# Optimization experiments

Measured on AMD Instinct MI355X. Metric: run time of the kernel, lower is better.

## Reference

```python
import jax, jax.numpy as jnp
import numpy as np

D_MODEL = 768
NUM_HEADS = 12
HEAD_DIM = D_MODEL // NUM_HEADS


def setup_inputs() -> dict:
    key = jax.random.key(0)
    ks = jax.random.split(key, 5)
    B, T = 2, 4096
    x = jax.random.normal(ks[0], (B, T, D_MODEL), dtype=jnp.float32)
    s_in = 1.0 / np.sqrt(D_MODEL)
    W_attn = jax.random.normal(ks[1], (D_MODEL, 3 * D_MODEL), dtype=jnp.float32) * s_in
    b_attn = jnp.zeros((3 * D_MODEL,), dtype=jnp.float32)
    W_proj = jax.random.normal(ks[2], (D_MODEL, D_MODEL), dtype=jnp.float32) * s_in
    b_proj = jnp.zeros((D_MODEL,), dtype=jnp.float32)
    return {"x": x, "W_attn": W_attn, "b_attn": b_attn, "W_proj": W_proj, "b_proj": b_proj}


def reference(x, W_attn, b_attn, W_proj, b_proj):
    B, T, C = x.shape
    H, D = NUM_HEADS, HEAD_DIM
    qkv = x @ W_attn + b_attn                      # [B,T,3C]
    q, k, v = jnp.split(qkv, 3, axis=-1)
    q = q.reshape(B, T, H, D).transpose(0, 2, 1, 3)  # [B,H,T,D]
    k = k.reshape(B, T, H, D).transpose(0, 2, 1, 3)
    v = v.reshape(B, T, H, D).transpose(0, 2, 1, 3)
    scores = jnp.einsum('bhqd,bhkd->bhqk', q, k) / jnp.sqrt(jnp.float32(D))
    attn = jax.nn.softmax(scores, axis=-1)          # [B,H,T,T]
    out = jnp.einsum('bhqk,bhkd->bhqd', attn, v)    # [B,H,T,D]
    out = out.transpose(0, 2, 1, 3).reshape(B, T, C)
    return out @ W_proj + b_proj
```

## Files before the change

### kernel.cpp

```cpp
#include <hip/hip_runtime.h>
#include <cstdint>
#include <cstddef>

#define DEV static __device__ __forceinline__

typedef __attribute__((ext_vector_type(8))) short bf16x8;
typedef __attribute__((ext_vector_type(4))) float f32x4;
typedef __attribute__((ext_vector_type(16))) float f32x16;

#define T_SEQ 4096
#define CDIM  768
#define NH    12
#define HD    64
#define NBH   24
#define M_ROWS 8192

#define OFF_XB   0ull
#define OFF_WAT  (OFF_XB  + (size_t)M_ROWS * CDIM * 2)
#define OFF_WPT  (OFF_WAT + (size_t)(3*CDIM) * CDIM * 2)
#define OFF_Q    (OFF_WPT + (size_t)CDIM * CDIM * 2)
#define OFF_K    (OFF_Q   + (size_t)NBH * T_SEQ * HD * 2)
#define OFF_VT   (OFF_K   + (size_t)NBH * T_SEQ * HD * 2)
#define OFF_O    (OFF_VT  + (size_t)NBH * HD * T_SEQ * 2)

DEV unsigned short f2bf(float f) {
  unsigned u = __builtin_bit_cast(unsigned, f);
  u += 0x7FFFu + ((u >> 16) & 1u);
  return (unsigned short)(u >> 16);
}

DEV void gld_lds16(const void* g, void* l) {
  __builtin_amdgcn_global_load_lds(
      (const __attribute__((address_space(1))) void*)g,
      (__attribute__((address_space(3))) void*)l, 16, 0, 0);
}

DEV void cvt8(const f32x16& s, unsigned* w) {
  asm("v_cvt_pk_bf16_f32 %0, %8, %9\n\t"
      "v_cvt_pk_bf16_f32 %1, %10, %11\n\t"
      "v_cvt_pk_bf16_f32 %2, %12, %13\n\t"
      "v_cvt_pk_bf16_f32 %3, %14, %15\n\t"
      "v_cvt_pk_bf16_f32 %4, %16, %17\n\t"
      "v_cvt_pk_bf16_f32 %5, %18, %19\n\t"
      "v_cvt_pk_bf16_f32 %6, %20, %21\n\t"
      "v_cvt_pk_bf16_f32 %7, %22, %23\n\t"
      "s_nop 3"
      : "=&v"(w[0]), "=&v"(w[1]), "=&v"(w[2]), "=&v"(w[3]),
        "=&v"(w[4]), "=&v"(w[5]), "=&v"(w[6]), "=&v"(w[7])
      : "v"(s[0]), "v"(s[1]), "v"(s[2]), "v"(s[3]),
        "v"(s[4]), "v"(s[5]), "v"(s[6]), "v"(s[7]),
        "v"(s[8]), "v"(s[9]), "v"(s[10]), "v"(s[11]),
        "v"(s[12]), "v"(s[13]), "v"(s[14]), "v"(s[15]));
}

__global__ __launch_bounds__(256) void k_conv(const float* __restrict__ in,
                                              unsigned short* __restrict__ out) {
  int i = blockIdx.x * 256 + threadIdx.x;
  const float4* p = (const float4*)in;
  float4 a = p[i * 2], b = p[i * 2 + 1];
  uint4 o;
  o.x = (unsigned)f2bf(a.x) | ((unsigned)f2bf(a.y) << 16);
  o.y = (unsigned)f2bf(a.z) | ((unsigned)f2bf(a.w) << 16);
  o.z = (unsigned)f2bf(b.x) | ((unsigned)f2bf(b.y) << 16);
  o.w = (unsigned)f2bf(b.z) | ((unsigned)f2bf(b.w) << 16);
  ((uint4*)out)[i] = o;
}

__global__ __launch_bounds__(256) void k_transpose(const float* __restrict__ in,
                                                   unsigned short* __restrict__ out,
                                                   int R, int C) {
  __shared__ float tile[64][65];
  int c0 = blockIdx.x * 64, r0 = blockIdx.y * 64;
  int tid = threadIdx.x;
  for (int i = tid; i < 4096; i += 256) {
    int r = i >> 6, c = i & 63;
    tile[r][c] = in[(size_t)(r0 + r) * C + c0 + c];
  }
  __syncthreads();
  for (int i = tid; i < 4096; i += 256) {
    int c = i >> 6, r = i & 63;
    out[(size_t)(c0 + c) * R + r0 + r] = f2bf(tile[r][c]);
  }
}

__global__ __launch_bounds__(256) void k_qkv(const unsigned short* __restrict__ A,
                                             const unsigned short* __restrict__ Bt,
                                             const float* __restrict__ bias,
                                             unsigned short* __restrict__ Qo,
                                             unsigned short* __restrict__ Ko,
                                             unsigned short* __restrict__ Vt) {
  __shared__ short As[128 * 64];
  __shared__ short Bs[128 * 64];
  const int tid = threadIdx.x;
  const int wave = tid >> 6, lane = tid & 63;
  const int wr = wave >> 1, wc = wave & 1;
  const int m0 = blockIdx.y * 128, n0 = blockIdx.x * 128;

  f32x4 acc[4][4] = {};

#pragma unroll 1
  for (int k0 = 0; k0 < 768; k0 += 64) {
#pragma unroll
    for (int it = 0; it < 4; ++it) {
      int chunk = wave * 4 + it;
      int slot = chunk * 64 + lane;
      int row = slot >> 3, j = slot & 7;
      int kcol = k0 + ((j ^ (row & 7)) << 3);
      gld_lds16(A  + (size_t)(m0 + row) * 768 + kcol, &As[chunk * 512]);
      gld_lds16(Bt + (size_t)(n0 + row) * 768 + kcol, &Bs[chunk * 512]);
    }
    __syncthreads();
#pragma unroll
    for (int kk = 0; kk < 2; ++kk) {
      bf16x8 af[4], bfr[4];
      int cbl = kk * 4 + (lane >> 4);
#pragma unroll
      for (int mi = 0; mi < 4; ++mi) {
        int row = wr * 64 + mi * 16 + (lane & 15);
        af[mi] = *(const bf16x8*)&As[(row * 8 + (cbl ^ (row & 7))) * 8];
      }
#pragma unroll
      for (int ni = 0; ni < 4; ++ni) {
        int row = wc * 64 + ni * 16 + (lane & 15);
        bfr[ni] = *(const bf16x8*)&Bs[(row * 8 + (cbl ^ (row & 7))) * 8];
      }
#pragma unroll
      for (int mi = 0; mi < 4; ++mi)
#pragma unroll
        for (int ni = 0; ni < 4; ++ni)
          acc[mi][ni] = __builtin_amdgcn_mfma_f32_16x16x32_bf16(af[mi], bfr[ni], acc[mi][ni], 0, 0, 0);
    }
    __syncthreads();
  }

  const int which = n0 / 768;
#pragma unroll
  for (int ni = 0; ni < 4; ++ni) {
    int col = n0 + wc * 64 + ni * 16 + (lane & 15);
    int nr = col - which * 768;
    int h = nr >> 6, d = nr & 63;
    float bi = bias[col];
#pragma unroll
    for (int mi = 0; mi < 4; ++mi) {
      int mt = m0 + wr * 64 + mi * 16 + ((lane >> 4) << 2);
      int b = mt >> 12, t = mt & 4095;
      size_t bh = (size_t)(b * NH + h);
#pragma unroll
      for (int r = 0; r < 4; ++r) {
        float v = acc[mi][ni][r] + bi;
        if (which == 0) {
          Qo[bh * (T_SEQ * HD) + (size_t)(t + r) * HD + d] = f2bf(v * 0.18033688011112042f);
        } else if (which == 1) {
          Ko[bh * (T_SEQ * HD) + (size_t)(t + r) * HD + d] = f2bf(v);
        } else {
          int tc = t + r;
          int pc = (tc & ~12) | ((tc & 4) << 1) | ((tc & 8) >> 1);
          Vt[bh * (T_SEQ * HD) + (size_t)d * T_SEQ + pc] = f2bf(v);
        }
      }
    }
  }
}

__global__ __launch_bounds__(256, 3) void k_attn(const unsigned short* __restrict__ Q,
                                                 const unsigned short* __restrict__ K,
                                                 const unsigned short* __restrict__ Vt,
                                                 unsigned short* __restrict__ O) {
  __shared__ char ldsb[2][16384];
  const int tid = threadIdx.x, wave = tid >> 6, lane = tid & 63;
  const int hi = lane >> 5, l31 = lane & 31;
  const int qt = blockIdx.x, bh = blockIdx.y;
  const int b = bh / NH, h = bh % NH;
  const size_t base = (size_t)bh * T_SEQ * HD;
  const int q0 = qt * 128 + wave * 32;

  bf16x8 aq[4];
#pragma unroll
  for (int t = 0; t < 4; ++t)
    aq[t] = *(const bf16x8*)&Q[base + (size_t)(q0 + l31) * HD + t * 16 + hi * 8];

  int koff[4];
#pragma unroll
  for (int t = 0; t < 4; ++t)
    koff[t] = l31 * 128 + ((((t << 1) | hi) ^ (l31 & 7)) << 4);
  int voff[2][2];
#pragma unroll
  for (int kb = 0; kb < 2; ++kb)
#pragma unroll
    for (int ks = 0; ks < 2; ++ks)
      voff[kb][ks] = ((((kb << 2) | (ks << 1) | hi) ^ (l31 & 7)) << 4) + l31 * 128;

  f32x16 oacc0 = {}, oacc1 = {}, lacc = {};
  union { unsigned u[4]; bf16x8 v; } onesf;
  onesf.u[0] = 0x3F803F80u; onesf.u[1] = 0x3F803F80u;
  onesf.u[2] = 0x3F803F80u; onesf.u[3] = 0x3F803F80u;

  auto STAGE = [&](int bufi, int k0) {
#pragma unroll
    for (int it = 0; it < 2; ++it) {
      int chunk = wave * 2 + it;
      int slot = chunk * 64 + lane;
      int row = slot >> 3, j = slot & 7;
      int ce = ((j ^ (row & 7)) << 3);
      gld_lds16(K  + base + (size_t)(k0 + row) * HD + ce, ldsb[bufi] + chunk * 1024);
      gld_lds16(Vt + base + (size_t)row * T_SEQ + k0 + ce, ldsb[bufi] + 8192 + chunk * 1024);
    }
  };

  STAGE(0, 0);
  __syncthreads();

  int buf = 0;
#pragma unroll 1
  for (int kt = 0; kt < 64; ++kt) {
    if (kt < 63) STAGE(buf ^ 1, (kt + 1) * 64);
    const char* Lp = ldsb[buf];
    const char* Vp = Lp + 8192;

    f32x16 s0 = {};
#pragma unroll
    for (int t = 0; t < 4; ++t) {
      bf16x8 kf = *(const bf16x8*)(Lp + koff[t]);
      s0 = __builtin_amdgcn_mfma_f32_32x32x16_bf16(kf, aq[t], s0, 0, 0, 0);
    }
#pragma unroll
    for (int r = 0; r < 16; ++r) s0[r] = __builtin_amdgcn_exp2f(s0[r]);
    unsigned w0[8];
    cvt8(s0, w0);
    union { unsigned u[4]; bf16x8 v; } pf00, pf01;
    pf00.u[0] = w0[0]; pf00.u[1] = w0[1]; pf00.u[2] = w0[2]; pf00.u[3] = w0[3];
    pf01.u[0] = w0[4]; pf01.u[1] = w0[5]; pf01.u[2] = w0[6]; pf01.u[3] = w0[7];

    f32x16 s1 = {};
#pragma unroll
    for (int t = 0; t < 4; ++t) {
      bf16x8 kf = *(const bf16x8*)(Lp + 4096 + koff[t]);
      s1 = __builtin_amdgcn_mfma_f32_32x32x16_bf16(kf, aq[t], s1, 0, 0, 0);
    }

    lacc = __builtin_amdgcn_mfma_f32_32x32x16_bf16(pf00.v, onesf.v, lacc, 0, 0, 0);
    lacc = __builtin_amdgcn_mfma_f32_32x32x16_bf16(pf01.v, onesf.v, lacc, 0, 0, 0);
    {
      bf16x8 v0 = *(const bf16x8*)(Vp + voff[0][0]);
      bf16x8 v1 = *(const bf16x8*)(Vp + voff[0][1]);
      bf16x8 u0 = *(const bf16x8*)(Vp + 4096 + voff[0][0]);
      bf16x8 u1 = *(const bf16x8*)(Vp + 4096 + voff[0][1]);
      oacc0 = __builtin_amdgcn_mfma_f32_32x32x16_bf16(pf00.v, v0, oacc0, 0, 0, 0);
      oacc0 = __builtin_amdgcn_mfma_f32_32x32x16_bf16(pf01.v, v1, oacc0, 0, 0, 0);
      oacc1 = __builtin_amdgcn_mfma_f32_32x32x16_bf16(pf00.v, u0, oacc1, 0, 0, 0);
      oacc1 = __builtin_amdgcn_mfma_f32_32x32x16_bf16(pf01.v, u1, oacc1, 0, 0, 0);
    }

#pragma unroll
    for (int r = 0; r < 16; ++r) s1[r] = __builtin_amdgcn_exp2f(s1[r]);
    unsigned w1[8];
    cvt8(s1, w1);
    union { unsigned u[4]; bf16x8 v; } pf10, pf11;
    pf10.u[0] = w1[0]; pf10.u[1] = w1[1]; pf10.u[2] = w1[2]; pf10.u[3] = w1[3];
    pf11.u[0] = w1[4]; pf11.u[1] = w1[5]; pf11.u[2] = w1[6]; pf11.u[3] = w1[7];

    lacc = __builtin_amdgcn_mfma_f32_32x32x16_bf16(pf10.v, onesf.v, lacc, 0, 0, 0);
    lacc = __builtin_amdgcn_mfma_f32_32x32x16_bf16(pf11.v, onesf.v, lacc, 0, 0, 0);
    {
      bf16x8 v0 = *(const bf16x8*)(Vp + voff[1][0]);
      bf16x8 v1 = *(const bf16x8*)(Vp + voff[1][1]);
      bf16x8 u0 = *(const bf16x8*)(Vp + 4096 + voff[1][0]);
      bf16x8 u1 = *(const bf16x8*)(Vp + 4096 + voff[1][1]);
      oacc0 = __builtin_amdgcn_mfma_f32_32x32x16_bf16(pf10.v, v0, oacc0, 0, 0, 0);
      oacc0 = __builtin_amdgcn_mfma_f32_32x32x16_bf16(pf11.v, v1, oacc0, 0, 0, 0);
      oacc1 = __builtin_amdgcn_mfma_f32_32x32x16_bf16(pf10.v, u0, oacc1, 0, 0, 0);
      oacc1 = __builtin_amdgcn_mfma_f32_32x32x16_bf16(pf11.v, u1, oacc1, 0, 0, 0);
    }

    __syncthreads();
    buf ^= 1;
  }

#pragma unroll
  for (int r = 0; r < 16; ++r) {
    float inv = 1.0f / lacc[r];
    int t = q0 + ((r & 3) + 8 * (r >> 2)) + 4 * hi;
    size_t rowb = (size_t)(b * T_SEQ + t) * CDIM + h * 64;
    O[rowb + l31]      = f2bf(oacc0[r] * inv);
    O[rowb + 32 + l31] = f2bf(oacc1[r] * inv);
  }
}

__global__ __launch_bounds__(256) void k_proj(const unsigned short* __restrict__ A,
                                              const unsigned short* __restrict__ Bt,
                                              const float* __restrict__ bias,
                                              float* __restrict__ out) {
  __shared__ short As[128 * 64];
  __shared__ short Bs[128 * 64];
  const int tid = threadIdx.x;
  const int wave = tid >> 6, lane = tid & 63;
  const int wr = wave >> 1, wc = wave & 1;
  const int m0 = blockIdx.y * 128, n0 = blockIdx.x * 128;

  f32x4 acc[4][4] = {};

#pragma unroll 1
  for (int k0 = 0; k0 < 768; k0 += 64) {
#pragma unroll
    for (int it = 0; it < 4; ++it) {
      int chunk = wave * 4 + it;
      int slot = chunk * 64 + lane;
      int row = slot >> 3, j = slot & 7;
      int kcol = k0 + ((j ^ (row & 7)) << 3);
      gld_lds16(A  + (size_t)(m0 + row) * 768 + kcol, &As[chunk * 512]);
      gld_lds16(Bt + (size_t)(n0 + row) * 768 + kcol, &Bs[chunk * 512]);
    }
    __syncthreads();
#pragma unroll
    for (int kk = 0; kk < 2; ++kk) {
      bf16x8 af[4], bfr[4];
      int cbl = kk * 4 + (lane >> 4);
#pragma unroll
      for (int mi = 0; mi < 4; ++mi) {
        int row = wr * 64 + mi * 16 + (lane & 15);
        af[mi] = *(const bf16x8*)&As[(row * 8 + (cbl ^ (row & 7))) * 8];
      }
#pragma unroll
      for (int ni = 0; ni < 4; ++ni) {
        int row = wc * 64 + ni * 16 + (lane & 15);
        bfr[ni] = *(const bf16x8*)&Bs[(row * 8 + (cbl ^ (row & 7))) * 8];
      }
#pragma unroll
      for (int mi = 0; mi < 4; ++mi)
#pragma unroll
        for (int ni = 0; ni < 4; ++ni)
          acc[mi][ni] = __builtin_amdgcn_mfma_f32_16x16x32_bf16(af[mi], bfr[ni], acc[mi][ni], 0, 0, 0);
    }
    __syncthreads();
  }

#pragma unroll
  for (int ni = 0; ni < 4; ++ni) {
    int col = n0 + wc * 64 + ni * 16 + (lane & 15);
    float bi = bias[col];
#pragma unroll
    for (int mi = 0; mi < 4; ++mi) {
      int mt = m0 + wr * 64 + mi * 16 + ((lane >> 4) << 2);
#pragma unroll
      for (int r = 0; r < 4; ++r)
        out[(size_t)(mt + r) * CDIM + col] = acc[mi][ni][r] + bi;
    }
  }
}

extern "C" void kernel_launch(void* const* d_in, const int* in_sizes, int n_in,
                              void* d_out, int out_size, void* d_ws, size_t ws_size,
                              hipStream_t stream) {
  const float* x  = (const float*)d_in[0];
  const float* Wa = (const float*)d_in[1];
  const float* ba = (const float*)d_in[2];
  const float* Wp = (const float*)d_in[3];
  const float* bp = (const float*)d_in[4];

  char* ws = (char*)d_ws;
  unsigned short* xb  = (unsigned short*)(ws + OFF_XB);
  unsigned short* WaT = (unsigned short*)(ws + OFF_WAT);
  unsigned short* WpT = (unsigned short*)(ws + OFF_WPT);
  unsigned short* Qb  = (unsigned short*)(ws + OFF_Q);
  unsigned short* Kb  = (unsigned short*)(ws + OFF_K);
  unsigned short* Vtb = (unsigned short*)(ws + OFF_VT);
  unsigned short* Ob  = (unsigned short*)(ws + OFF_O);

  k_conv<<<3072, 256, 0, stream>>>(x, xb);
  k_transpose<<<dim3(36, 12), 256, 0, stream>>>(Wa, WaT, CDIM, 3 * CDIM);
  k_transpose<<<dim3(12, 12), 256, 0, stream>>>(Wp, WpT, CDIM, CDIM);
  k_qkv<<<dim3(18, 64), 256, 0, stream>>>(xb, WaT, ba, Qb, Kb, Vtb);
  k_attn<<<dim3(32, 24), 256, 0, stream>>>(Qb, Kb, Vtb, Ob);
  k_proj<<<dim3(6, 64), 256, 0, stream>>>(Ob, WpT, bp, (float*)d_out);
}
```

Baseline: 229.5 us.

## Replace MFMA row-sum with VALU sum and remap workgroups per XCD

In the attention kernel, the softmax denominator was computed with extra MFMA instructions that multiplied P by a ones vector. It is now a per-lane scalar sum of the exponentials, combined with a cross-lane shuffle at the end, which removes four MFMAs per iteration in exchange for some VALU adds. Separately, all three kernels remap the linear block index so that consecutive blocks land on the same XCD (eight-way interleave), to improve L2 reuse of shared K/V and weight tiles. The remapping assumes the grid sizes are divisible by 8, and the sum now uses fp32 values rather than the bf16-rounded P that the PV product uses.

```diff
diff --git a/kernel.cpp b/kernel.cpp
--- a/kernel.cpp
+++ b/kernel.cpp
@@ -94,7 +94,9 @@
   const int tid = threadIdx.x;
   const int wave = tid >> 6, lane = tid & 63;
   const int wr = wave >> 1, wc = wave & 1;
-  const int m0 = blockIdx.y * 128, n0 = blockIdx.x * 128;
+  const int lin = blockIdx.y * 18 + blockIdx.x;
+  const int wg = (lin & 7) * 144 + (lin >> 3);
+  const int m0 = (wg / 18) * 128, n0 = (wg % 18) * 128;
 
   f32x4 acc[4][4] = {};
 
@@ -169,7 +171,9 @@
   __shared__ char ldsb[2][16384];
   const int tid = threadIdx.x, wave = tid >> 6, lane = tid & 63;
   const int hi = lane >> 5, l31 = lane & 31;
-  const int qt = blockIdx.x, bh = blockIdx.y;
+  const int lin = blockIdx.y * 32 + blockIdx.x;
+  const int wg = (lin & 7) * 96 + (lin >> 3);
+  const int qt = wg & 31, bh = wg >> 5;
   const int b = bh / NH, h = bh % NH;
   const size_t base = (size_t)bh * T_SEQ * HD;
   const int q0 = qt * 128 + wave * 32;
@@ -190,10 +194,8 @@
     for (int ks = 0; ks < 2; ++ks)
       voff[kb][ks] = ((((kb << 2) | (ks << 1) | hi) ^ (l31 & 7)) << 4) + l31 * 128;
 
-  f32x16 oacc0 = {}, oacc1 = {}, lacc = {};
-  union { unsigned u[4]; bf16x8 v; } onesf;
-  onesf.u[0] = 0x3F803F80u; onesf.u[1] = 0x3F803F80u;
-  onesf.u[2] = 0x3F803F80u; onesf.u[3] = 0x3F803F80u;
+  f32x16 oacc0 = {}, oacc1 = {};
+  float l = 0.f;
 
   auto STAGE = [&](int bufi, int k0) {
 #pragma unroll
@@ -225,6 +227,13 @@
     }
 #pragma unroll
     for (int r = 0; r < 16; ++r) s0[r] = __builtin_amdgcn_exp2f(s0[r]);
+    {
+      float a8[8];
+#pragma unroll
+      for (int i = 0; i < 8; ++i) a8[i] = s0[2 * i] + s0[2 * i + 1];
+      float a4a = a8[0] + a8[1], a4b = a8[2] + a8[3], a4c = a8[4] + a8[5], a4d = a8[6] + a8[7];
+      l += (a4a + a4b) + (a4c + a4d);
+    }
     unsigned w0[8];
     cvt8(s0, w0);
     union { unsigned u[4]; bf16x8 v; } pf00, pf01;
@@ -238,8 +247,6 @@
       s1 = __builtin_amdgcn_mfma_f32_32x32x16_bf16(kf, aq[t], s1, 0, 0, 0);
     }
 
-    lacc = __builtin_amdgcn_mfma_f32_32x32x16_bf16(pf00.v, onesf.v, lacc, 0, 0, 0);
-    lacc = __builtin_amdgcn_mfma_f32_32x32x16_bf16(pf01.v, onesf.v, lacc, 0, 0, 0);
     {
       bf16x8 v0 = *(const bf16x8*)(Vp + voff[0][0]);
       bf16x8 v1 = *(const bf16x8*)(Vp + voff[0][1]);
@@ -253,14 +260,19 @@
 
 #pragma unroll
     for (int r = 0; r < 16; ++r) s1[r] = __builtin_amdgcn_exp2f(s1[r]);
+    {
+      float a8[8];
+#pragma unroll
+      for (int i = 0; i < 8; ++i) a8[i] = s1[2 * i] + s1[2 * i + 1];
+      float a4a = a8[0] + a8[1], a4b = a8[2] + a8[3], a4c = a8[4] + a8[5], a4d = a8[6] + a8[7];
+      l += (a4a + a4b) + (a4c + a4d);
+    }
     unsigned w1[8];
     cvt8(s1, w1);
     union { unsigned u[4]; bf16x8 v; } pf10, pf11;
     pf10.u[0] = w1[0]; pf10.u[1] = w1[1]; pf10.u[2] = w1[2]; pf10.u[3] = w1[3];
     pf11.u[0] = w1[4]; pf11.u[1] = w1[5]; pf11.u[2] = w1[6]; pf11.u[3] = w1[7];
 
-    lacc = __builtin_amdgcn_mfma_f32_32x32x16_bf16(pf10.v, onesf.v, lacc, 0, 0, 0);
-    lacc = __builtin_amdgcn_mfma_f32_32x32x16_bf16(pf11.v, onesf.v, lacc, 0, 0, 0);
     {
       bf16x8 v0 = *(const bf16x8*)(Vp + voff[1][0]);
       bf16x8 v1 = *(const bf16x8*)(Vp + voff[1][1]);
@@ -276,9 +288,12 @@
     buf ^= 1;
   }
 
+  l += __shfl_xor(l, 32, 64);
+
 #pragma unroll
   for (int r = 0; r < 16; ++r) {
-    float inv = 1.0f / lacc[r];
+    float lt = __shfl(l, ((r & 3) + 8 * (r >> 2)) + 4 * hi, 64);
+    float inv = 1.0f / lt;
     int t = q0 + ((r & 3) + 8 * (r >> 2)) + 4 * hi;
     size_t rowb = (size_t)(b * T_SEQ + t) * CDIM + h * 64;
     O[rowb + l31]      = f2bf(oacc0[r] * inv);
@@ -295,7 +310,9 @@
   const int tid = threadIdx.x;
   const int wave = tid >> 6, lane = tid & 63;
   const int wr = wave >> 1, wc = wave & 1;
-  const int m0 = blockIdx.y * 128, n0 = blockIdx.x * 128;
+  const int lin = blockIdx.y * 6 + blockIdx.x;
+  const int wg = (lin & 7) * 48 + (lin >> 3);
+  const int m0 = (wg / 6) * 128, n0 = (wg % 6) * 128;
 
   f32x4 acc[4][4] = {};
 
```

New measurement: 222.9 us. 1.03x faster.
